# Performance work log

Measured on AMD Instinct MI355X. Metric: run time of the kernel, lower is better.

The kernel has to match this reference:

```python
import jax, jax.numpy as jnp
import numpy as np

H = 16          # n_heads
D_MODEL = 1024
DK = D_MODEL // H  # 64
N = 2048        # total tokens (module flattens batch*seq)
NEG = -1000000000.0


def setup_inputs() -> dict:
    key = jax.random.key(0)
    ks = jax.random.split(key, 12)
    s = 1.0 / np.sqrt(D_MODEL)
    inp = {
        "query": jax.random.normal(ks[0], (N, D_MODEL), jnp.float32),
        "key": jax.random.normal(ks[1], (N, D_MODEL), jnp.float32),
        "value": jax.random.normal(ks[2], (N, D_MODEL), jnp.float32),
        "mask": jax.random.randint(ks[3], (1, N), 0, 2, jnp.int32),
        "Wq": jax.random.normal(ks[4], (D_MODEL, D_MODEL), jnp.float32) * s,
        "bq": jax.random.normal(ks[5], (D_MODEL,), jnp.float32) * 0.01,
        "Wk": jax.random.normal(ks[6], (D_MODEL, D_MODEL), jnp.float32) * s,
        "bk": jax.random.normal(ks[7], (D_MODEL,), jnp.float32) * 0.01,
        "Wv": jax.random.normal(ks[8], (D_MODEL, D_MODEL), jnp.float32) * s,
        "bv": jax.random.normal(ks[9], (D_MODEL,), jnp.float32) * 0.01,
        "Wo": jax.random.normal(ks[10], (D_MODEL, D_MODEL), jnp.float32) * s,
        "bo": jax.random.normal(ks[11], (D_MODEL,), jnp.float32) * 0.01,
    }
    return inp


def reference(query, key, value, mask, Wq, bq, Wk, bk, Wv, bv, Wo, bo):
    # Linear projections (torch Linear: x @ W.T + b), then split heads: (N, d_model) -> (h, N, d_k)
    def split_heads(x):
        return x.reshape(-1, H, DK).transpose(1, 0, 2)

    q = split_heads(query @ Wq.T + bq)
    k = split_heads(key @ Wk.T + bk)
    v = split_heads(value @ Wv.T + bv)

    # scaled dot-product attention: scores (h, N, N)
    scores = jnp.einsum("hnd,hmd->hnm", q, k) / jnp.sqrt(jnp.asarray(DK, q.dtype))
    # mask: (1, N) --unsqueeze(1)--> (1, 1, N), broadcast over (h, N, N)
    scores = jnp.where(mask[None, :, :] == 0, jnp.asarray(NEG, scores.dtype), scores)
    p_attn = jax.nn.softmax(scores, axis=-1)  # dropout identity (eval mode)

    x = jnp.einsum("hnm,hmd->hnd", p_attn, v)  # (h, N, d_k)
    x = x.transpose(1, 0, 2).reshape(-1, H * DK)  # (N, d_model)
    out = x @ Wo.T + bo
    return (out, p_attn)
```

## Files before the change

kernel.cpp:

```cpp
#include <hip/hip_runtime.h>


#define NTOK 2048
#define DMODEL 1024
#define NHEAD 16
#define DKH 64

typedef __attribute__((ext_vector_type(8))) short bf16x8;
typedef __attribute__((ext_vector_type(4))) float f32x4;
typedef __attribute__((ext_vector_type(16))) float f32x16;

#define WAITVMC(n)                                          \
  do {                                                      \
    asm volatile("s_waitcnt vmcnt(" n ")" ::: "memory");    \
    __builtin_amdgcn_sched_barrier(0);                      \
  } while (0)
#define BARRIER()                                           \
  do {                                                      \
    __builtin_amdgcn_s_barrier();                           \
    __builtin_amdgcn_sched_barrier(0);                      \
  } while (0)

__device__ __forceinline__ unsigned short f2bf(float x) {
  unsigned int u = __builtin_bit_cast(unsigned int, x);
  u += 0x7fffu + ((u >> 16) & 1u);
  return (unsigned short)(u >> 16);
}
__device__ __forceinline__ unsigned int pkbf(float a, float b) {
  return (unsigned int)f2bf(a) | ((unsigned int)f2bf(b) << 16);
}

__device__ __forceinline__ void gl16(const void* g, void* l) {
  __builtin_amdgcn_global_load_lds((const __attribute__((address_space(1))) void*)g,
                                   (__attribute__((address_space(3))) void*)l, 16, 0, 0);
}

template<int ROWS, int NW>
__device__ __forceinline__ void stage_async(const unsigned short* src, int ld,
                                            char* lds, int w, int lane) {
  constexpr int RPW = ROWS / NW;
#pragma unroll
  for (int i = 0; i < RPW / 8; ++i) {
    const int row = w * RPW + i * 8 + (lane >> 3);
    const unsigned short* g = src + (size_t)row * ld + (((lane & 7) ^ (row & 7)) * 8);
    gl16(g, lds + (size_t)(w * RPW + i * 8) * 128);
  }
}

__device__ __forceinline__ bf16x8 ldsfrag(const char* lds, int r, int kb) {
  return *(const bf16x8*)(lds + r * 128 + (kb ^ ((r & 7) << 4)));
}

struct CvtP {
  const float* src[7];
  unsigned short* dst[7];
  int n8[8];
  const int* mask;
  float* mbias;
};
__global__ __launch_bounds__(256) void cvt_all(CvtP P) {
  const int a = blockIdx.z;
  const int i = blockIdx.x * 256 + threadIdx.x;
  if (i >= P.n8[a]) return;
  if (a == 7) {
#pragma unroll
    for (int r = 0; r < 8; ++r) {
      int j = i * 8 + r;
      P.mbias[j] = P.mask[j] ? 0.0f : -1e30f;
    }
    return;
  }
  const float4* s = (const float4*)P.src[a];
  float4 v0 = s[i * 2], v1 = s[i * 2 + 1];
  ushort4 h0, h1;
  h0.x = f2bf(v0.x); h0.y = f2bf(v0.y); h0.z = f2bf(v0.z); h0.w = f2bf(v0.w);
  h1.x = f2bf(v1.x); h1.y = f2bf(v1.y); h1.z = f2bf(v1.z); h1.w = f2bf(v1.w);
  ((ushort4*)P.dst[a])[i * 2] = h0;
  ((ushort4*)P.dst[a])[i * 2 + 1] = h1;
}

struct GemmP2 {
  const unsigned short* A[3];
  const unsigned short* B[3];
  const float* bias[3];
  unsigned short* Cb16;
  float* Cf32;
  unsigned short* VTd;
  long long sC;
  int lda, ldb, ldc, Nn, K;
};

template<int BM, int BN, bool OUTF32, bool VTRANS>
__global__ __launch_bounds__(256) void gemm_glds(GemmP2 P) {
  constexpr int WN = BN / 2, FN = WN / 16;
  constexpr int WM = BM / 2, FM = WM / 16;
  __shared__ char ldsA[BM * 128];
  __shared__ char ldsB[BN * 128];
  const int tid = threadIdx.x;
  const int lane = tid & 63, w = tid >> 6;
  const int l15 = lane & 15, lhi = lane >> 4;
  const int z = blockIdx.z;
  const int zi = (gridDim.z == 3) ? z : 0;
  const int ntn = P.Nn / BN;
  const int m0 = ((int)blockIdx.x / ntn) * BM;
  const int n0 = ((int)blockIdx.x % ntn) * BN;
  const unsigned short* Ab = P.A[zi] + (size_t)m0 * P.lda;
  const unsigned short* Bb = P.B[zi] + (size_t)n0 * P.ldb;
  const int wm = w >> 1, wn = w & 1;

  f32x4 acc[FM][FN] = {};
  for (int k0 = 0; k0 < P.K; k0 += 64) {
    stage_async<BM, 4>(Ab + k0, P.lda, ldsA, w, lane);
    stage_async<BN, 4>(Bb + k0, P.ldb, ldsB, w, lane);
    __syncthreads();
#pragma unroll
    for (int kk = 0; kk < 2; ++kk) {
      const int kb = kk * 64 + lhi * 16;
      bf16x8 a[FM], b[FN];
#pragma unroll
      for (int i = 0; i < FM; ++i) a[i] = ldsfrag(ldsA, wm * WM + i * 16 + l15, kb);
#pragma unroll
      for (int j = 0; j < FN; ++j) b[j] = ldsfrag(ldsB, wn * WN + j * 16 + l15, kb);
#pragma unroll
      for (int i = 0; i < FM; ++i)
#pragma unroll
        for (int j = 0; j < FN; ++j)
          acc[i][j] = __builtin_amdgcn_mfma_f32_16x16x32_bf16(a[i], b[j], acc[i][j], 0, 0, 0);
    }
    __syncthreads();
  }

  const int rbase = m0 + wm * WM + lhi * 4;
  const int cbase = n0 + wn * WN + l15;
  if (VTRANS && z == 2) {
#pragma unroll
    for (int j = 0; j < FN; ++j) {
      const int col = cbase + j * 16;
      const float badd = P.bias[zi][col];
#pragma unroll
      for (int i = 0; i < FM; ++i) {
        ushort4 t;
        t.x = f2bf(acc[i][j][0] + badd); t.y = f2bf(acc[i][j][1] + badd);
        t.z = f2bf(acc[i][j][2] + badd); t.w = f2bf(acc[i][j][3] + badd);
        *(ushort4*)(P.VTd + (size_t)col * NTOK + rbase + i * 16) = t;
      }
    }
    return;
  }
#pragma unroll
  for (int j = 0; j < FN; ++j) {
    const int col = cbase + j * 16;
    const float badd = P.bias[zi] ? P.bias[zi][col] : 0.0f;
#pragma unroll
    for (int i = 0; i < FM; ++i) {
#pragma unroll
      for (int rg = 0; rg < 4; ++rg) {
        const int row = rbase + i * 16 + rg;
        const float v = acc[i][j][rg] + badd;
        if constexpr (OUTF32)
          P.Cf32[(size_t)row * P.ldc + col] = v;
        else
          P.Cb16[(size_t)z * P.sC + (size_t)row * P.ldc + col] = f2bf(v);
      }
    }
  }
}

__global__ __launch_bounds__(256, 2) void attn8(const unsigned short* __restrict__ QP,
                                                const unsigned short* __restrict__ KP,
                                                const unsigned short* __restrict__ VT,
                                                const float* __restrict__ mbias,
                                                float* __restrict__ p,
                                                unsigned short* __restrict__ XB) {
  __shared__ char LDS[81920];
  const int tid = threadIdx.x;
  const int lane = tid & 63, w = tid >> 6;
  const int rg = w >> 1, jg = w & 1;
  const int m31 = lane & 31, hi = lane >> 5;
  const int id = blockIdx.x;
  const int h = 2 * (id & 7) + ((id >> 3) & 1);
  const int q0 = (id >> 4) * 64;
  const int row_q = rg * 32 + m31;
  const int swq = (row_q & 7) << 4;
  const int swm = (m31 & 7) << 4;
  constexpr float CEXP = 0.1803368801111204f;

  char* ldsKb[2] = {LDS + jg * 16384, LDS + jg * 16384 + 8192};
  char* ldsVb[2] = {LDS + 32768 + jg * 16384, LDS + 32768 + jg * 16384 + 8192};
  char* ldsPj = LDS + 65536 + jg * 8192;
  char* ldsQ = LDS + 65536;
  float* ldsR = (float*)(LDS + 65536 + 8192);

  stage_async<64, 4>(QP + (size_t)q0 * DMODEL + h * DKH, DMODEL, ldsQ, w, lane);
  __syncthreads();
  bf16x8 qf[4];
#pragma unroll
  for (int kt = 0; kt < 4; ++kt)
    qf[kt] = *(const bf16x8*)(ldsQ + row_q * 128 + ((kt * 32 + hi * 16) ^ swq));

  const unsigned short* Kh = KP + (size_t)(jg * 1024) * DMODEL + h * DKH;
  const unsigned short* Vh = VT + (size_t)h * DKH * NTOK + jg * 1024;
  const float* mbh = mbias + jg * 1024;

  float rsum = 0.0f;
  float4 m4[8];
  stage_async<64, 2>(Kh, DMODEL, ldsKb[0], rg, lane);
#pragma unroll
  for (int q = 0; q < 8; ++q)
    m4[q] = *(const float4*)(mbh + (q >> 2) * 32 + (q & 3) * 8 + hi * 4);
  int b = 0;
  for (int it = 0; it < 16; ++it) {
    WAITVMC("8");
    BARRIER();
    if (it < 15)
      stage_async<64, 2>(Kh + (size_t)(it + 1) * 64 * DMODEL, DMODEL, ldsKb[b ^ 1], rg, lane);
    __builtin_amdgcn_sched_barrier(0);
    f32x16 s0 = {}, s1 = {};
    __builtin_amdgcn_s_setprio(1);
#pragma unroll
    for (int kt = 0; kt < 4; ++kt) {
      bf16x8 k0 = *(const bf16x8*)(ldsKb[b] + m31 * 128 + ((kt * 32 + hi * 16) ^ swm));
      bf16x8 k1 = *(const bf16x8*)(ldsKb[b] + (32 + m31) * 128 + ((kt * 32 + hi * 16) ^ swm));
      s0 = __builtin_amdgcn_mfma_f32_32x32x16_bf16(k0, qf[kt], s0, 0, 0, 0);
      s1 = __builtin_amdgcn_mfma_f32_32x32x16_bf16(k1, qf[kt], s1, 0, 0, 0);
    }
    __builtin_amdgcn_s_setprio(0);
#pragma unroll
    for (int rq = 0; rq < 4; ++rq) {
      rsum += exp2f(s0[rq * 4 + 0] * CEXP + m4[rq].x) + exp2f(s0[rq * 4 + 1] * CEXP + m4[rq].y) +
              exp2f(s0[rq * 4 + 2] * CEXP + m4[rq].z) + exp2f(s0[rq * 4 + 3] * CEXP + m4[rq].w);
      rsum += exp2f(s1[rq * 4 + 0] * CEXP + m4[4 + rq].x) + exp2f(s1[rq * 4 + 1] * CEXP + m4[4 + rq].y) +
              exp2f(s1[rq * 4 + 2] * CEXP + m4[4 + rq].z) + exp2f(s1[rq * 4 + 3] * CEXP + m4[4 + rq].w);
    }
    if (it < 15) {
      const float* mb2 = mbh + (it + 1) * 64;
#pragma unroll
      for (int q = 0; q < 8; ++q)
        m4[q] = *(const float4*)(mb2 + (q >> 2) * 32 + (q & 3) * 8 + hi * 4);
    }
    b ^= 1;
  }
  rsum += __shfl_xor(rsum, 32, 64);
  if (lane < 32) ldsR[jg * 64 + row_q] = rsum;
  BARRIER();
  const float lr = -log2f(ldsR[row_q] + ldsR[64 + row_q]);

  f32x16 x0 = {}, x1 = {};
  stage_async<64, 2>(Kh, DMODEL, ldsKb[0], rg, lane);
  stage_async<64, 2>(Vh, NTOK, ldsVb[0], rg, lane);
#pragma unroll
  for (int q = 0; q < 8; ++q)
    m4[q] = *(const float4*)(mbh + (q >> 2) * 32 + (q & 3) * 8 + hi * 4);
  b = 0;
  for (int it = 0; it < 16; ++it) {
    const int j0 = it * 64;
    if (it == 0) { WAITVMC("8"); } else { WAITVMC("16"); }
    BARRIER();
    if (it < 15) {
      stage_async<64, 2>(Kh + (size_t)(j0 + 64) * DMODEL, DMODEL, ldsKb[b ^ 1], rg, lane);
      stage_async<64, 2>(Vh + j0 + 64, NTOK, ldsVb[b ^ 1], rg, lane);
    }
    __builtin_amdgcn_sched_barrier(0);
    f32x16 s0 = {}, s1 = {};
    __builtin_amdgcn_s_setprio(1);
#pragma unroll
    for (int kt = 0; kt < 4; ++kt) {
      bf16x8 k0 = *(const bf16x8*)(ldsKb[b] + m31 * 128 + ((kt * 32 + hi * 16) ^ swm));
      bf16x8 k1 = *(const bf16x8*)(ldsKb[b] + (32 + m31) * 128 + ((kt * 32 + hi * 16) ^ swm));
      s0 = __builtin_amdgcn_mfma_f32_32x32x16_bf16(k0, qf[kt], s0, 0, 0, 0);
      s1 = __builtin_amdgcn_mfma_f32_32x32x16_bf16(k1, qf[kt], s1, 0, 0, 0);
    }
    __builtin_amdgcn_s_setprio(0);
#pragma unroll
    for (int rq = 0; rq < 4; ++rq) {
      uint2 u;
      u.x = pkbf(exp2f(s0[rq * 4 + 0] * CEXP + m4[rq].x + lr),
                 exp2f(s0[rq * 4 + 1] * CEXP + m4[rq].y + lr));
      u.y = pkbf(exp2f(s0[rq * 4 + 2] * CEXP + m4[rq].z + lr),
                 exp2f(s0[rq * 4 + 3] * CEXP + m4[rq].w + lr));
      *(uint2*)(ldsPj + row_q * 128 + ((rq * 16 + hi * 8) ^ swq)) = u;
      uint2 v;
      v.x = pkbf(exp2f(s1[rq * 4 + 0] * CEXP + m4[4 + rq].x + lr),
                 exp2f(s1[rq * 4 + 1] * CEXP + m4[4 + rq].y + lr));
      v.y = pkbf(exp2f(s1[rq * 4 + 2] * CEXP + m4[4 + rq].z + lr),
                 exp2f(s1[rq * 4 + 3] * CEXP + m4[4 + rq].w + lr));
      *(uint2*)(ldsPj + row_q * 128 + ((64 + rq * 16 + hi * 8) ^ swq)) = v;
    }
    __builtin_amdgcn_s_setprio(1);
#pragma unroll
    for (int ks = 0; ks < 4; ++ks) {
      bf16x8 pf = *(const bf16x8*)(ldsPj + row_q * 128 + ((ks * 32 + hi * 16) ^ swq));
      bf16x8 v0 = *(const bf16x8*)(ldsVb[b] + m31 * 128 + ((ks * 32 + hi * 16) ^ swm));
      bf16x8 v1 = *(const bf16x8*)(ldsVb[b] + (32 + m31) * 128 + ((ks * 32 + hi * 16) ^ swm));
      x0 = __builtin_amdgcn_mfma_f32_32x32x16_bf16(v0, pf, x0, 0, 0, 0);
      x1 = __builtin_amdgcn_mfma_f32_32x32x16_bf16(v1, pf, x1, 0, 0, 0);
    }
    __builtin_amdgcn_s_setprio(0);
    if (it < 15) {
      const float* mb2 = mbh + (j0 + 64);
#pragma unroll
      for (int q = 0; q < 8; ++q)
        m4[q] = *(const float4*)(mb2 + (q >> 2) * 32 + (q & 3) * 8 + hi * 4);
    }
    float* pb = p + ((size_t)h * NTOK + q0) * NTOK + jg * 1024 + j0;
#pragma unroll
    for (int rb = 0; rb < 4; ++rb) {
      const int rr = rg * 32 + rb * 8 + (lane >> 3);
      const int swr = (rr & 7) << 4;
#pragma unroll
      for (int hh = 0; hh < 2; ++hh) {
        const uint2 u = *(const uint2*)(ldsPj + rr * 128 + ((((lane & 7) * 8) + hh * 64) ^ swr));
        f32x4 f;
        f[0] = __builtin_bit_cast(float, u.x << 16);
        f[1] = __builtin_bit_cast(float, u.x & 0xffff0000u);
        f[2] = __builtin_bit_cast(float, u.y << 16);
        f[3] = __builtin_bit_cast(float, u.y & 0xffff0000u);
        __builtin_nontemporal_store(f, (f32x4*)(pb + (size_t)rr * NTOK + hh * 32 + (lane & 7) * 4));
      }
    }
    b ^= 1;
  }

  float* ldsX = (float*)LDS;
  BARRIER();
  if (jg == 1) {
#pragma unroll
    for (int db = 0; db < 2; ++db) {
      const f32x16 xx = db ? x1 : x0;
#pragma unroll
      for (int rq = 0; rq < 4; ++rq) {
        f32x4 v;
        v[0] = xx[rq * 4 + 0]; v[1] = xx[rq * 4 + 1];
        v[2] = xx[rq * 4 + 2]; v[3] = xx[rq * 4 + 3];
        *(f32x4*)((char*)ldsX + row_q * 256 + ((db * 128 + rq * 32 + hi * 16) ^ swq)) = v;
      }
    }
  }
  BARRIER();
  if (jg == 0) {
    unsigned short* xr = XB + (size_t)(q0 + row_q) * DMODEL + h * DKH;
#pragma unroll
    for (int db = 0; db < 2; ++db) {
      const f32x16 xx = db ? x1 : x0;
#pragma unroll
      for (int rq = 0; rq < 4; ++rq) {
        f32x4 o = *(const f32x4*)((char*)ldsX + row_q * 256 + ((db * 128 + rq * 32 + hi * 16) ^ swq));
        o[0] += xx[rq * 4 + 0]; o[1] += xx[rq * 4 + 1];
        o[2] += xx[rq * 4 + 2]; o[3] += xx[rq * 4 + 3];
        ushort4 t;
        t.x = f2bf(o[0]); t.y = f2bf(o[1]); t.z = f2bf(o[2]); t.w = f2bf(o[3]);
        *(ushort4*)(xr + db * 32 + rq * 8 + hi * 4) = t;
      }
    }
  }
}

extern "C" void kernel_launch(void* const* d_in, const int* in_sizes, int n_in,
                              void* d_out, int out_size, void* d_ws, size_t ws_size,
                              hipStream_t stream) {
  (void)in_sizes; (void)n_in; (void)out_size; (void)ws_size;
  const float* query = (const float*)d_in[0];
  const float* key_  = (const float*)d_in[1];
  const float* value = (const float*)d_in[2];
  const int*   mask  = (const int*)d_in[3];
  const float* Wq = (const float*)d_in[4];
  const float* bq = (const float*)d_in[5];
  const float* Wk = (const float*)d_in[6];
  const float* bk = (const float*)d_in[7];
  const float* Wv = (const float*)d_in[8];
  const float* bv = (const float*)d_in[9];
  const float* Wo = (const float*)d_in[10];
  const float* bo = (const float*)d_in[11];

  float* out = (float*)d_out;
  float* p = out + (size_t)NTOK * DMODEL;

  char* ws = (char*)d_ws;
  unsigned short* QP  = (unsigned short*)(ws);
  unsigned short* KP  = (unsigned short*)(ws + (4u << 20));
  unsigned short* VT  = (unsigned short*)(ws + (8u << 20));
  unsigned short* XB  = (unsigned short*)(ws + (12u << 20));
  unsigned short* qB  = (unsigned short*)(ws + (16u << 20));
  unsigned short* kB  = (unsigned short*)(ws + (20u << 20));
  unsigned short* vB  = (unsigned short*)(ws + (24u << 20));
  unsigned short* WqB = (unsigned short*)(ws + (28u << 20));
  unsigned short* WkB = (unsigned short*)(ws + (30u << 20));
  unsigned short* WvB = (unsigned short*)(ws + (32u << 20));
  unsigned short* WoB = (unsigned short*)(ws + (34u << 20));
  float* mbias = (float*)(ws + (36u << 20));

  {
    CvtP C = {};
    C.src[0] = query; C.dst[0] = qB;  C.n8[0] = NTOK * DMODEL / 8;
    C.src[1] = key_;  C.dst[1] = kB;  C.n8[1] = NTOK * DMODEL / 8;
    C.src[2] = value; C.dst[2] = vB;  C.n8[2] = NTOK * DMODEL / 8;
    C.src[3] = Wq;    C.dst[3] = WqB; C.n8[3] = DMODEL * DMODEL / 8;
    C.src[4] = Wk;    C.dst[4] = WkB; C.n8[4] = DMODEL * DMODEL / 8;
    C.src[5] = Wv;    C.dst[5] = WvB; C.n8[5] = DMODEL * DMODEL / 8;
    C.src[6] = Wo;    C.dst[6] = WoB; C.n8[6] = DMODEL * DMODEL / 8;
    C.n8[7] = NTOK / 8;
    C.mask = mask; C.mbias = mbias;
    cvt_all<<<dim3(1024, 1, 8), 256, 0, stream>>>(C);
  }
  {
    GemmP2 P = {};
    P.A[0] = qB; P.A[1] = kB; P.A[2] = vB;
    P.B[0] = WqB; P.B[1] = WkB; P.B[2] = WvB;
    P.bias[0] = bq; P.bias[1] = bk; P.bias[2] = bv;
    P.Cb16 = QP; P.VTd = VT; P.sC = (long long)NTOK * DMODEL;
    P.lda = DMODEL; P.ldb = DMODEL; P.ldc = DMODEL; P.Nn = DMODEL; P.K = DMODEL;
    gemm_glds<64, 128, false, true>
        <<<dim3((NTOK / 64) * (DMODEL / 128), 1, 3), 256, 0, stream>>>(P);
  }
  attn8<<<dim3(512), 256, 0, stream>>>(QP, KP, VT, mbias, p, XB);
  {
    GemmP2 P = {};
    P.A[0] = XB; P.B[0] = WoB; P.bias[0] = bo;
    P.Cf32 = out; P.sC = 0;
    P.lda = DMODEL; P.ldb = DMODEL; P.ldc = DMODEL; P.Nn = DMODEL; P.K = DMODEL;
    gemm_glds<64, 64, true, false>
        <<<dim3((NTOK / 64) * (DMODEL / 64), 1, 1), 256, 0, stream>>>(P);
  }
}
```

Measured before the change: 146.2 us.

## Split attention into row-sum and PV kernels, pack mask into bitmasks

The fused attention kernel is split in two. A lighter row-sum kernel (smaller LDS, launch bounds allowing 4 blocks per CU) computes the softmax log-normaliser and writes it to global memory. A second kernel reads that normaliser and does P·V plus the p_attn store. The float mask-bias array is replaced by 64-bit bitmasks that select exp values, which removes the per-iteration float4 mask loads and the registers they held. The cost is an extra kernel launch, a second Q load and a small global round-trip for the normalisers.

```diff
diff --git a/kernel.cpp b/kernel.cpp
--- a/kernel.cpp
+++ b/kernel.cpp
@@ -56,18 +56,18 @@
   unsigned short* dst[7];
   int n8[8];
   const int* mask;
-  float* mbias;
+  unsigned long long* mbits;
 };
 __global__ __launch_bounds__(256) void cvt_all(CvtP P) {
   const int a = blockIdx.z;
   const int i = blockIdx.x * 256 + threadIdx.x;
   if (i >= P.n8[a]) return;
   if (a == 7) {
-#pragma unroll
-    for (int r = 0; r < 8; ++r) {
-      int j = i * 8 + r;
-      P.mbias[j] = P.mask[j] ? 0.0f : -1e30f;
-    }
+    unsigned long long bset = 0;
+#pragma unroll 8
+    for (int k = 0; k < 64; ++k)
+      bset |= (unsigned long long)(P.mask[i * 64 + k] != 0) << k;
+    P.mbits[i] = bset;
     return;
   }
   const float4* s = (const float4*)P.src[a];
@@ -166,12 +166,83 @@
   }
 }
 
-__global__ __launch_bounds__(256, 2) void attn8(const unsigned short* __restrict__ QP,
-                                                const unsigned short* __restrict__ KP,
-                                                const unsigned short* __restrict__ VT,
-                                                const float* __restrict__ mbias,
-                                                float* __restrict__ p,
-                                                unsigned short* __restrict__ XB) {
+__global__ __launch_bounds__(256, 4) void attn_rsum(const unsigned short* __restrict__ QP,
+                                                    const unsigned short* __restrict__ KP,
+                                                    const unsigned long long* __restrict__ mbits,
+                                                    float* __restrict__ lrg) {
+  __shared__ char LDS[40960];
+  const int tid = threadIdx.x;
+  const int lane = tid & 63, w = tid >> 6;
+  const int rg = w >> 1, jg = w & 1;
+  const int m31 = lane & 31, hi = lane >> 5;
+  const int id = blockIdx.x;
+  const int h = 2 * (id & 7) + ((id >> 3) & 1);
+  const int q0 = (id >> 4) * 64;
+  const int row_q = rg * 32 + m31;
+  const int swq = (row_q & 7) << 4;
+  const int swm = (m31 & 7) << 4;
+  constexpr float CEXP = 0.1803368801111204f;
+
+  char* ldsKb[2] = {LDS + jg * 16384, LDS + jg * 16384 + 8192};
+  char* ldsQ = LDS + 32768;
+
+  stage_async<64, 4>(QP + (size_t)q0 * DMODEL + h * DKH, DMODEL, ldsQ, w, lane);
+  __syncthreads();
+  bf16x8 qf[4];
+#pragma unroll
+  for (int kt = 0; kt < 4; ++kt)
+    qf[kt] = *(const bf16x8*)(ldsQ + row_q * 128 + ((kt * 32 + hi * 16) ^ swq));
+
+  const unsigned short* Kh = KP + (size_t)(jg * 1024) * DMODEL + h * DKH;
+  float rsum = 0.0f;
+  stage_async<64, 2>(Kh, DMODEL, ldsKb[0], rg, lane);
+  int b = 0;
+  for (int it = 0; it < 16; ++it) {
+    WAITVMC("0");
+    BARRIER();
+    const unsigned long long bits = mbits[jg * 16 + it];
+    if (it < 15)
+      stage_async<64, 2>(Kh + (size_t)(it + 1) * 64 * DMODEL, DMODEL, ldsKb[b ^ 1], rg, lane);
+    __builtin_amdgcn_sched_barrier(0);
+    f32x16 s0 = {}, s1 = {};
+    __builtin_amdgcn_s_setprio(1);
+#pragma unroll
+    for (int kt = 0; kt < 4; ++kt) {
+      bf16x8 k0 = *(const bf16x8*)(ldsKb[b] + m31 * 128 + ((kt * 32 + hi * 16) ^ swm));
+      bf16x8 k1 = *(const bf16x8*)(ldsKb[b] + (32 + m31) * 128 + ((kt * 32 + hi * 16) ^ swm));
+      s0 = __builtin_amdgcn_mfma_f32_32x32x16_bf16(k0, qf[kt], s0, 0, 0, 0);
+      s1 = __builtin_amdgcn_mfma_f32_32x32x16_bf16(k1, qf[kt], s1, 0, 0, 0);
+    }
+    __builtin_amdgcn_s_setprio(0);
+    const unsigned long long bs = bits >> (hi * 4);
+#pragma unroll
+    for (int rq = 0; rq < 4; ++rq) {
+#pragma unroll
+      for (int e = 0; e < 4; ++e) {
+        const float e0 = exp2f(s0[rq * 4 + e] * CEXP);
+        rsum += ((bs >> (rq * 8 + e)) & 1) ? e0 : 0.0f;
+        const float e1 = exp2f(s1[rq * 4 + e] * CEXP);
+        rsum += ((bs >> (rq * 8 + e + 32)) & 1) ? e1 : 0.0f;
+      }
+    }
+    b ^= 1;
+  }
+  rsum += __shfl_xor(rsum, 32, 64);
+  float* ldsR = (float*)ldsQ;
+  BARRIER();
+  if (lane < 32) ldsR[jg * 64 + row_q] = rsum;
+  BARRIER();
+  if (jg == 0 && lane < 32)
+    lrg[(size_t)h * NTOK + q0 + row_q] = -log2f(ldsR[row_q] + ldsR[64 + row_q]);
+}
+
+__global__ __launch_bounds__(256, 2) void attn_pv(const unsigned short* __restrict__ QP,
+                                                  const unsigned short* __restrict__ KP,
+                                                  const unsigned short* __restrict__ VT,
+                                                  const unsigned long long* __restrict__ mbits,
+                                                  const float* __restrict__ lrg,
+                                                  float* __restrict__ p,
+                                                  unsigned short* __restrict__ XB) {
   __shared__ char LDS[81920];
   const int tid = threadIdx.x;
   const int lane = tid & 63, w = tid >> 6;
@@ -189,7 +260,8 @@
   char* ldsVb[2] = {LDS + 32768 + jg * 16384, LDS + 32768 + jg * 16384 + 8192};
   char* ldsPj = LDS + 65536 + jg * 8192;
   char* ldsQ = LDS + 65536;
-  float* ldsR = (float*)(LDS + 65536 + 8192);
+
+  const float lr = lrg[(size_t)h * NTOK + q0 + row_q];
 
   stage_async<64, 4>(QP + (size_t)q0 * DMODEL + h * DKH, DMODEL, ldsQ, w, lane);
   __syncthreads();
@@ -197,23 +269,24 @@
 #pragma unroll
   for (int kt = 0; kt < 4; ++kt)
     qf[kt] = *(const bf16x8*)(ldsQ + row_q * 128 + ((kt * 32 + hi * 16) ^ swq));
+  __syncthreads();
 
   const unsigned short* Kh = KP + (size_t)(jg * 1024) * DMODEL + h * DKH;
   const unsigned short* Vh = VT + (size_t)h * DKH * NTOK + jg * 1024;
-  const float* mbh = mbias + jg * 1024;
-
-  float rsum = 0.0f;
-  float4 m4[8];
+
+  f32x16 x0 = {}, x1 = {};
   stage_async<64, 2>(Kh, DMODEL, ldsKb[0], rg, lane);
-#pragma unroll
-  for (int q = 0; q < 8; ++q)
-    m4[q] = *(const float4*)(mbh + (q >> 2) * 32 + (q & 3) * 8 + hi * 4);
+  stage_async<64, 2>(Vh, NTOK, ldsVb[0], rg, lane);
   int b = 0;
   for (int it = 0; it < 16; ++it) {
-    WAITVMC("8");
+    const int j0 = it * 64;
+    if (it == 0) { WAITVMC("0"); } else { WAITVMC("8"); }
     BARRIER();
-    if (it < 15)
-      stage_async<64, 2>(Kh + (size_t)(it + 1) * 64 * DMODEL, DMODEL, ldsKb[b ^ 1], rg, lane);
+    const unsigned long long bits = mbits[jg * 16 + it];
+    if (it < 15) {
+      stage_async<64, 2>(Kh + (size_t)(j0 + 64) * DMODEL, DMODEL, ldsKb[b ^ 1], rg, lane);
+      stage_async<64, 2>(Vh + j0 + 64, NTOK, ldsVb[b ^ 1], rg, lane);
+    }
     __builtin_amdgcn_sched_barrier(0);
     f32x16 s0 = {}, s1 = {};
     __builtin_amdgcn_s_setprio(1);
@@ -225,65 +298,22 @@
       s1 = __builtin_amdgcn_mfma_f32_32x32x16_bf16(k1, qf[kt], s1, 0, 0, 0);
     }
     __builtin_amdgcn_s_setprio(0);
+    const unsigned long long bs = bits >> (hi * 4);
 #pragma unroll
     for (int rq = 0; rq < 4; ++rq) {
-      rsum += exp2f(s0[rq * 4 + 0] * CEXP + m4[rq].x) + exp2f(s0[rq * 4 + 1] * CEXP + m4[rq].y) +
-              exp2f(s0[rq * 4 + 2] * CEXP + m4[rq].z) + exp2f(s0[rq * 4 + 3] * CEXP + m4[rq].w);
-      rsum += exp2f(s1[rq * 4 + 0] * CEXP + m4[4 + rq].x) + exp2f(s1[rq * 4 + 1] * CEXP + m4[4 + rq].y) +
-              exp2f(s1[rq * 4 + 2] * CEXP + m4[4 + rq].z) + exp2f(s1[rq * 4 + 3] * CEXP + m4[4 + rq].w);
-    }
-    if (it < 15) {
-      const float* mb2 = mbh + (it + 1) * 64;
-#pragma unroll
-      for (int q = 0; q < 8; ++q)
-        m4[q] = *(const float4*)(mb2 + (q >> 2) * 32 + (q & 3) * 8 + hi * 4);
-    }
-    b ^= 1;
-  }
-  rsum += __shfl_xor(rsum, 32, 64);
-  if (lane < 32) ldsR[jg * 64 + row_q] = rsum;
-  BARRIER();
-  const float lr = -log2f(ldsR[row_q] + ldsR[64 + row_q]);
-
-  f32x16 x0 = {}, x1 = {};
-  stage_async<64, 2>(Kh, DMODEL, ldsKb[0], rg, lane);
-  stage_async<64, 2>(Vh, NTOK, ldsVb[0], rg, lane);
-#pragma unroll
-  for (int q = 0; q < 8; ++q)
-    m4[q] = *(const float4*)(mbh + (q >> 2) * 32 + (q & 3) * 8 + hi * 4);
-  b = 0;
-  for (int it = 0; it < 16; ++it) {
-    const int j0 = it * 64;
-    if (it == 0) { WAITVMC("8"); } else { WAITVMC("16"); }
-    BARRIER();
-    if (it < 15) {
-      stage_async<64, 2>(Kh + (size_t)(j0 + 64) * DMODEL, DMODEL, ldsKb[b ^ 1], rg, lane);
-      stage_async<64, 2>(Vh + j0 + 64, NTOK, ldsVb[b ^ 1], rg, lane);
-    }
-    __builtin_amdgcn_sched_barrier(0);
-    f32x16 s0 = {}, s1 = {};
-    __builtin_amdgcn_s_setprio(1);
-#pragma unroll
-    for (int kt = 0; kt < 4; ++kt) {
-      bf16x8 k0 = *(const bf16x8*)(ldsKb[b] + m31 * 128 + ((kt * 32 + hi * 16) ^ swm));
-      bf16x8 k1 = *(const bf16x8*)(ldsKb[b] + (32 + m31) * 128 + ((kt * 32 + hi * 16) ^ swm));
-      s0 = __builtin_amdgcn_mfma_f32_32x32x16_bf16(k0, qf[kt], s0, 0, 0, 0);
-      s1 = __builtin_amdgcn_mfma_f32_32x32x16_bf16(k1, qf[kt], s1, 0, 0, 0);
-    }
-    __builtin_amdgcn_s_setprio(0);
-#pragma unroll
-    for (int rq = 0; rq < 4; ++rq) {
+      float e0[4], e1[4];
+#pragma unroll
+      for (int e = 0; e < 4; ++e) {
+        const float t0 = exp2f(s0[rq * 4 + e] * CEXP + lr);
+        e0[e] = ((bs >> (rq * 8 + e)) & 1) ? t0 : 0.0f;
+        const float t1 = exp2f(s1[rq * 4 + e] * CEXP + lr);
+        e1[e] = ((bs >> (rq * 8 + e + 32)) & 1) ? t1 : 0.0f;
+      }
       uint2 u;
-      u.x = pkbf(exp2f(s0[rq * 4 + 0] * CEXP + m4[rq].x + lr),
-                 exp2f(s0[rq * 4 + 1] * CEXP + m4[rq].y + lr));
-      u.y = pkbf(exp2f(s0[rq * 4 + 2] * CEXP + m4[rq].z + lr),
-                 exp2f(s0[rq * 4 + 3] * CEXP + m4[rq].w + lr));
+      u.x = pkbf(e0[0], e0[1]); u.y = pkbf(e0[2], e0[3]);
       *(uint2*)(ldsPj + row_q * 128 + ((rq * 16 + hi * 8) ^ swq)) = u;
       uint2 v;
-      v.x = pkbf(exp2f(s1[rq * 4 + 0] * CEXP + m4[4 + rq].x + lr),
-                 exp2f(s1[rq * 4 + 1] * CEXP + m4[4 + rq].y + lr));
-      v.y = pkbf(exp2f(s1[rq * 4 + 2] * CEXP + m4[4 + rq].z + lr),
-                 exp2f(s1[rq * 4 + 3] * CEXP + m4[4 + rq].w + lr));
+      v.x = pkbf(e1[0], e1[1]); v.y = pkbf(e1[2], e1[3]);
       *(uint2*)(ldsPj + row_q * 128 + ((64 + rq * 16 + hi * 8) ^ swq)) = v;
     }
     __builtin_amdgcn_s_setprio(1);
@@ -296,12 +326,6 @@
       x1 = __builtin_amdgcn_mfma_f32_32x32x16_bf16(v1, pf, x1, 0, 0, 0);
     }
     __builtin_amdgcn_s_setprio(0);
-    if (it < 15) {
-      const float* mb2 = mbh + (j0 + 64);
-#pragma unroll
-      for (int q = 0; q < 8; ++q)
-        m4[q] = *(const float4*)(mb2 + (q >> 2) * 32 + (q & 3) * 8 + hi * 4);
-    }
     float* pb = p + ((size_t)h * NTOK + q0) * NTOK + jg * 1024 + j0;
 #pragma unroll
     for (int rb = 0; rb < 4; ++rb) {
@@ -387,7 +411,8 @@
   unsigned short* WkB = (unsigned short*)(ws + (30u << 20));
   unsigned short* WvB = (unsigned short*)(ws + (32u << 20));
   unsigned short* WoB = (unsigned short*)(ws + (34u << 20));
-  float* mbias = (float*)(ws + (36u << 20));
+  float* lrg = (float*)(ws + (36u << 20));
+  unsigned long long* mbits = (unsigned long long*)(ws + (37u << 20));
 
   {
     CvtP C = {};
@@ -398,8 +423,8 @@
     C.src[4] = Wk;    C.dst[4] = WkB; C.n8[4] = DMODEL * DMODEL / 8;
     C.src[5] = Wv;    C.dst[5] = WvB; C.n8[5] = DMODEL * DMODEL / 8;
     C.src[6] = Wo;    C.dst[6] = WoB; C.n8[6] = DMODEL * DMODEL / 8;
-    C.n8[7] = NTOK / 8;
-    C.mask = mask; C.mbias = mbias;
+    C.n8[7] = NTOK / 64;
+    C.mask = mask; C.mbits = mbits;
     cvt_all<<<dim3(1024, 1, 8), 256, 0, stream>>>(C);
   }
   {
@@ -412,7 +437,8 @@
     gemm_glds<64, 128, false, true>
         <<<dim3((NTOK / 64) * (DMODEL / 128), 1, 3), 256, 0, stream>>>(P);
   }
-  attn8<<<dim3(512), 256, 0, stream>>>(QP, KP, VT, mbias, p, XB);
+  attn_rsum<<<dim3(512), 256, 0, stream>>>(QP, KP, mbits, lrg);
+  attn_pv<<<dim3(512), 256, 0, stream>>>(QP, KP, VT, mbits, lrg, p, XB);
   {
     GemmP2 P = {};
     P.A[0] = XB; P.B[0] = WoB; P.bias[0] = bo;
```

New measurement: 153.1 us. 4.7% more time.
